# Performance work log

Hardware: AMD Instinct MI355X
Metric: run time of the kernel (lower is better)

The kernel has to match this reference:

```python
import jax, jax.numpy as jnp
import numpy as np
import math

V, BS, D, L, H = 50257, 1024, 768, 12, 4
DH = D // H  # 192
B, T = 4, 1024


def setup_inputs() -> dict:
    key = jax.random.key(0)
    ks = jax.random.split(key, 18)
    s = 0.02
    inp = {
        "x": jax.random.randint(ks[0], (B, T), 0, V),
        "tok_emb": jax.random.normal(ks[1], (V, D), jnp.float32) * s,
        "pos_emb": jax.random.normal(ks[2], (BS, D), jnp.float32) * s,
        "ln1_s": jnp.ones((L, D), jnp.float32),
        "ln1_b": jnp.zeros((L, D), jnp.float32),
        "qkv_w": jax.random.normal(ks[3], (L, D, 3 * D), jnp.float32) * s,
        "qkv_b": jnp.zeros((L, 3 * D), jnp.float32),
        "ln2_s": jnp.ones((L, D), jnp.float32),
        "ln2_b": jnp.zeros((L, D), jnp.float32),
        "fc_w": jax.random.normal(ks[4], (L, D, 4 * D), jnp.float32) * s,
        "fc_b": jnp.zeros((L, 4 * D), jnp.float32),
        "proj_w": jax.random.normal(ks[5], (L, 4 * D, D), jnp.float32) * s,
        "proj_b": jnp.zeros((L, D), jnp.float32),
        "lnf_s": jnp.ones((D,), jnp.float32),
        "lnf_b": jnp.zeros((D,), jnp.float32),
        "head_w": jax.random.normal(ks[6], (D, V), jnp.float32) * s,
        "head_b": jnp.zeros((V,), jnp.float32),
    }
    return inp


def _ln(x, scale, shift):
    m = x.mean(-1, keepdims=True)
    v = jnp.mean((x - m) ** 2, axis=-1, keepdims=True)
    return (x - m) * jax.lax.rsqrt(v + 1e-5) * scale + shift


def _forward(x, tok_emb, pos_emb, ln1_s, ln1_b, qkv_w, qkv_b, ln2_s, ln2_b,
             fc_w, fc_b, proj_w, proj_b, lnf_s, lnf_b, head_w, head_b):
    Bx, Tx = x.shape
    h = tok_emb[x] + pos_emb[:Tx]  # [B,T,D]
    causal = jnp.tril(jnp.ones((Tx, Tx), bool))
    scale = 1.0 / math.sqrt(DH)

    def block(h, p):
        s1, b1, wq, bq, s2, b2, wf, bf, wp, bp = p
        # attention (no output projection, faithful to source)
        ln1 = _ln(h, s1, b1)
        qkv = ln1 @ wq + bq  # [B,T,3D]
        q, k, v = jnp.split(qkv, 3, axis=-1)
        q = q.reshape(Bx, Tx, H, DH)
        k = k.reshape(Bx, Tx, H, DH)
        v = v.reshape(Bx, Tx, H, DH)
        att = jnp.einsum('bthd,bshd->bhts', q, k) * scale
        att = jnp.where(causal, att, -jnp.inf)
        att = jax.nn.softmax(att, axis=-1)
        y = jnp.einsum('bhts,bshd->bthd', att, v).reshape(Bx, Tx, D)
        h = h + y
        # MLP (ReLU, despite attr named gelu in source)
        ln2 = _ln(h, s2, b2)
        m = jax.nn.relu(ln2 @ wf + bf) @ wp + bp
        return h + m, None

    h, _ = jax.lax.scan(block, h,
                        (ln1_s, ln1_b, qkv_w, qkv_b, ln2_s, ln2_b,
                         fc_w, fc_b, proj_w, proj_b))
    h = _ln(h, lnf_s, lnf_b)
    return h @ head_w + head_b  # [B,T,V]


def reference(x, tok_emb, pos_emb, ln1_s, ln1_b, qkv_w, qkv_b, ln2_s, ln2_b,
              fc_w, fc_b, proj_w, proj_b, lnf_s, lnf_b, head_w, head_b):
    return _forward(x, tok_emb, pos_emb, ln1_s, ln1_b, qkv_w, qkv_b,
                    ln2_s, ln2_b, fc_w, fc_b, proj_w, proj_b,
                    lnf_s, lnf_b, head_w, head_b)
```

## Files before the change

### kernel.cpp

```cpp
#include <hip/hip_runtime.h>
#include <stdint.h>

#define D_MODEL 768
#define NHEAD 4
#define DHEAD 192
#define SEQ 1024
#define NLAYER 12
#define NTOK 4096
#define NVOCAB 50257

typedef __attribute__((ext_vector_type(4))) float f32x4;
typedef __attribute__((ext_vector_type(4))) int i32x4;
typedef __attribute__((ext_vector_type(4))) unsigned short u16x4;

__device__ __forceinline__ unsigned short f2bf(float f) {
  unsigned u = __builtin_bit_cast(unsigned, f);
  u += 0x7FFFu + ((u >> 16) & 1u);
  return (unsigned short)(u >> 16);
}

#define GLDS(src, dst)                                                   \
  __builtin_amdgcn_global_load_lds(                                      \
      (const __attribute__((address_space(1))) void*)(src),              \
      (__attribute__((address_space(3))) void*)(dst), 16, 0, 0)

__global__ __launch_bounds__(256) void embed_kernel(
    const int* __restrict__ x, const float* __restrict__ tok,
    const float* __restrict__ pos, float* __restrict__ h) {
  int row = blockIdx.x;
  int t = row & (SEQ - 1);
  int id = x[row];
  const float* tp = tok + (long)id * D_MODEL;
  const float* pp = pos + (long)t * D_MODEL;
  float* hp = h + (long)row * D_MODEL;
  for (int j = threadIdx.x; j < D_MODEL; j += 256)
    hp[j] = tp[j] + pp[j];
}

__global__ __launch_bounds__(256) void ln_kernel(
    const float* __restrict__ h, const float* __restrict__ sc,
    const float* __restrict__ sh, unsigned short* __restrict__ out) {
  __shared__ float red[4];
  int row = blockIdx.x;
  const float* x = h + (long)row * D_MODEL;
  int tid = threadIdx.x;
  float v0 = x[tid], v1 = x[tid + 256], v2 = x[tid + 512];
  float s = v0 + v1 + v2;
  for (int o = 32; o > 0; o >>= 1) s += __shfl_xor(s, o);
  if ((tid & 63) == 0) red[tid >> 6] = s;
  __syncthreads();
  float mean = (red[0] + red[1] + red[2] + red[3]) * (1.0f / D_MODEL);
  __syncthreads();
  float d0 = v0 - mean, d1 = v1 - mean, d2 = v2 - mean;
  float q = d0 * d0 + d1 * d1 + d2 * d2;
  for (int o = 32; o > 0; o >>= 1) q += __shfl_xor(q, o);
  if ((tid & 63) == 0) red[tid >> 6] = q;
  __syncthreads();
  float var = (red[0] + red[1] + red[2] + red[3]) * (1.0f / D_MODEL);
  float r = rsqrtf(var + 1e-5f);
  unsigned short* op = out + (long)row * D_MODEL;
  op[tid]       = f2bf(d0 * r * sc[tid]       + sh[tid]);
  op[tid + 256] = f2bf(d1 * r * sc[tid + 256] + sh[tid + 256]);
  op[tid + 512] = f2bf(d2 * r * sc[tid + 512] + sh[tid + 512]);
}

__global__ __launch_bounds__(256) void wtrans_kernel(
    const float* __restrict__ w, unsigned short* __restrict__ wt, int K, int N) {
  __shared__ unsigned short tile[32][33];
  int n0 = blockIdx.x * 32, k0 = blockIdx.y * 32;
  int tx = threadIdx.x, ty = threadIdx.y;
  int n = n0 + tx; if (n >= N) n = N - 1;
  #pragma unroll
  for (int i = 0; i < 4; ++i) {
    int k = k0 + ty + i * 8;
    tile[ty + i * 8][tx] = f2bf(w[(long)k * N + n]);
  }
  __syncthreads();
  #pragma unroll
  for (int i = 0; i < 4; ++i) {
    int nn = n0 + ty + i * 8;
    if (nn < N) wt[(long)nn * K + k0 + tx] = tile[tx][ty + i * 8];
  }
}

__global__ __launch_bounds__(256) void vt_kernel(
    const unsigned short* __restrict__ qkv, unsigned short* __restrict__ vt) {
  __shared__ unsigned short tile[32][33];
  int bh = blockIdx.z, b = bh >> 2, hh = bh & 3;
  int t0 = blockIdx.x * 32, f0 = blockIdx.y * 32;
  int tx = threadIdx.x, ty = threadIdx.y;
  const unsigned short* src = qkv + (long)b * SEQ * 2304 + 2 * D_MODEL + hh * DHEAD;
  #pragma unroll
  for (int i = 0; i < 4; ++i) {
    int t = t0 + ty + i * 8;
    tile[ty + i * 8][tx] = src[(long)t * 2304 + f0 + tx];
  }
  __syncthreads();
  unsigned short* dst = vt + (long)bh * DHEAD * SEQ;
  #pragma unroll
  for (int i = 0; i < 4; ++i) {
    int f = f0 + ty + i * 8;
    dst[(long)f * SEQ + t0 + tx] = tile[tx][ty + i * 8];
  }
}

__global__ __launch_bounds__(256) void softmax_kernel(
    const float* __restrict__ S, unsigned short* __restrict__ P) {
  __shared__ float red[4];
  long rid = blockIdx.x;
  int q = (int)(rid & (SEQ - 1));
  int tid = threadIdx.x;
  int i0 = tid * 4;
  f32x4 v = *(const f32x4*)(S + rid * SEQ + i0);
  float m = -3.0e38f;
  #pragma unroll
  for (int j = 0; j < 4; ++j) {
    if (i0 + j > q) v[j] = -3.0e38f;
    m = fmaxf(m, v[j]);
  }
  for (int o = 32; o > 0; o >>= 1) m = fmaxf(m, __shfl_xor(m, o));
  if ((tid & 63) == 0) red[tid >> 6] = m;
  __syncthreads();
  m = fmaxf(fmaxf(red[0], red[1]), fmaxf(red[2], red[3]));
  __syncthreads();
  float e[4];
  float sum = 0.f;
  #pragma unroll
  for (int j = 0; j < 4; ++j) {
    e[j] = (i0 + j > q) ? 0.f : __expf(v[j] - m);
    sum += e[j];
  }
  for (int o = 32; o > 0; o >>= 1) sum += __shfl_xor(sum, o);
  if ((tid & 63) == 0) red[tid >> 6] = sum;
  __syncthreads();
  float inv = 1.0f / (red[0] + red[1] + red[2] + red[3]);
  u16x4 out;
  #pragma unroll
  for (int j = 0; j < 4; ++j) out[j] = f2bf(e[j] * inv);
  *(u16x4*)(P + rid * SEQ + i0) = out;
}

#define BM 128
#define BN 128
#define BKK 32

template<int MODE>
__global__ __launch_bounds__(256) void gemm_kernel(
    const unsigned short* __restrict__ A, int lda,
    const unsigned short* __restrict__ B, int ldb,
    const float* __restrict__ bias,
    void* __restrict__ Cv, int ldc,
    int M, int N, int K,
    int NI, long sAo, long sAi, long sBo, long sBi,
    long sCo, long sCi, float alpha, int causal, int mblocks) {
  __shared__ __align__(16) unsigned short As[BM * BKK];
  __shared__ __align__(16) unsigned short Bs[BN * BKK];
  int z = blockIdx.z;
  int zo = z / NI, zi = z - zo * NI;
  A += zo * sAo + zi * sAi;
  B += zo * sBo + zi * sBi;
  long coff = zo * sCo + zi * sCi;

  int m0, n0;
  if (mblocks > 0) {
    int bid = blockIdx.x;
    int qq = (int)gridDim.x >> 3;
    bid = (bid & 7) * qq + (bid >> 3);
    m0 = (bid % mblocks) * BM;
    n0 = (bid / mblocks) * BN;
  } else {
    m0 = blockIdx.y * BM;
    n0 = blockIdx.x * BN;
  }
  if (causal == 1 && n0 > m0 + BM - 1) return;
  int kmax = (causal == 2) ? min(K, m0 + BM) : K;

  int tid = threadIdx.x;
  int lane = tid & 63;
  int wave = tid >> 6;
  int wm = (wave >> 1) * 64;
  int wn = (wave & 1) * 64;

  f32x4 acc[4][4] = {};

  for (int k0 = 0; k0 < kmax; k0 += BKK) {
    __syncthreads();
    #pragma unroll
    for (int i = 0; i < 2; ++i) {
      int c0 = i * 256 + wave * 64;
      int cc = c0 + lane;
      int row = cc >> 2;
      int ko = (cc & 3) << 3;
      GLDS(A + (long)(m0 + row) * lda + k0 + ko, As + c0 * 8);
      int rg = n0 + row; if (rg >= N) rg = N - 1;
      GLDS(B + (long)rg * ldb + k0 + ko, Bs + c0 * 8);
    }
    __syncthreads();
    int lr = lane & 15;
    int kg = (lane >> 4) << 3;
    i32x4 af[4], bf[4];
    #pragma unroll
    for (int mi = 0; mi < 4; ++mi)
      af[mi] = *(const i32x4*)(As + (wm + mi * 16 + lr) * BKK + kg);
    #pragma unroll
    for (int ni = 0; ni < 4; ++ni)
      bf[ni] = *(const i32x4*)(Bs + (wn + ni * 16 + lr) * BKK + kg);
    #pragma unroll
    for (int mi = 0; mi < 4; ++mi)
      #pragma unroll
      for (int ni = 0; ni < 4; ++ni)
        asm("v_mfma_f32_16x16x32_bf16 %0, %1, %2, %0"
            : "+v"(acc[mi][ni]) : "v"(af[mi]), "v"(bf[ni]));
  }

  int cr = (lane >> 4) << 2;
  int cn = lane & 15;
  #pragma unroll
  for (int mi = 0; mi < 4; ++mi) {
    #pragma unroll
    for (int ni = 0; ni < 4; ++ni) {
      int col = n0 + wn + ni * 16 + cn;
      if (col >= N) continue;
      float bv = (MODE == 2) ? 0.f : (bias ? bias[col] : 0.f);
      #pragma unroll
      for (int r = 0; r < 4; ++r) {
        long row = m0 + wm + mi * 16 + cr + r;
        float v = acc[mi][ni][r] * alpha + bv;
        long idx = coff + row * ldc + col;
        if (MODE == 0)      ((unsigned short*)Cv)[idx] = f2bf(v);
        else if (MODE == 1) ((unsigned short*)Cv)[idx] = f2bf(fmaxf(v, 0.f));
        else if (MODE == 2) ((float*)Cv)[idx] = v;
        else if (MODE == 3) ((float*)Cv)[idx] += v;
        else                ((float*)Cv)[idx] = v;
      }
    }
  }
}

extern "C" void kernel_launch(void* const* d_in, const int* in_sizes, int n_in,
                              void* d_out, int out_size, void* d_ws, size_t ws_size,
                              hipStream_t stream) {
  const int*   x       = (const int*)  d_in[0];
  const float* tok_emb = (const float*)d_in[1];
  const float* pos_emb = (const float*)d_in[2];
  const float* ln1_s   = (const float*)d_in[3];
  const float* ln1_b   = (const float*)d_in[4];
  const float* qkv_w   = (const float*)d_in[5];
  const float* qkv_b   = (const float*)d_in[6];
  const float* ln2_s   = (const float*)d_in[7];
  const float* ln2_b   = (const float*)d_in[8];
  const float* fc_w    = (const float*)d_in[9];
  const float* fc_b    = (const float*)d_in[10];
  const float* proj_w  = (const float*)d_in[11];
  const float* proj_b  = (const float*)d_in[12];
  const float* lnf_s   = (const float*)d_in[13];
  const float* lnf_b   = (const float*)d_in[14];
  const float* head_w  = (const float*)d_in[15];
  const float* head_b  = (const float*)d_in[16];

  char* ws = (char*)d_ws;
  size_t off = 0;
  auto alloc = [&](size_t bytes) {
    char* p = ws + off;
    off += (bytes + 255) & ~(size_t)255;
    return p;
  };
  float*          h   = (float*)         alloc((size_t)NTOK * D_MODEL * 4);
  unsigned short* lnb = (unsigned short*)alloc((size_t)NTOK * D_MODEL * 2);
  unsigned short* qkv = (unsigned short*)alloc((size_t)NTOK * 2304 * 2);
  unsigned short* vt  = (unsigned short*)alloc((size_t)16 * DHEAD * SEQ * 2);
  unsigned short* mid = (unsigned short*)alloc((size_t)NTOK * 3072 * 2);
  float*          S   = (float*)         alloc((size_t)16 * SEQ * SEQ * 4);
  unsigned short* P   = (unsigned short*)alloc((size_t)16 * SEQ * SEQ * 2);
  unsigned short* wtq = (unsigned short*)alloc((size_t)2304 * 768 * 2);
  unsigned short* wtf = (unsigned short*)alloc((size_t)3072 * 768 * 2);
  unsigned short* wtp = (unsigned short*)alloc((size_t)768 * 3072 * 2);
  unsigned short* wth = (unsigned short*)alloc((size_t)50304 * 768 * 2);

  embed_kernel<<<NTOK, 256, 0, stream>>>(x, tok_emb, pos_emb, h);

  const float rscale = 0.07216878364870323f;

  for (int l = 0; l < NLAYER; ++l) {
    wtrans_kernel<<<dim3(72, 24), dim3(32, 8), 0, stream>>>(
        qkv_w + (long)l * 768 * 2304, wtq, 768, 2304);
    ln_kernel<<<NTOK, 256, 0, stream>>>(h, ln1_s + l * 768, ln1_b + l * 768, lnb);
    gemm_kernel<0><<<dim3(18, 32, 1), 256, 0, stream>>>(
        lnb, 768, wtq, 768, qkv_b + l * 2304, qkv, 2304,
        4096, 2304, 768, 1, 0, 0, 0, 0, 0, 0, 1.0f, 0, 0);
    vt_kernel<<<dim3(32, 6, 16), dim3(32, 8), 0, stream>>>(qkv, vt);
    gemm_kernel<2><<<dim3(8, 8, 16), 256, 0, stream>>>(
        qkv, 2304, qkv + 768, 2304, nullptr, S, 1024,
        1024, 1024, 192, 4,
        (long)1024 * 2304, 192, (long)1024 * 2304, 192,
        (long)4 * 1024 * 1024, (long)1024 * 1024, rscale, 1, 0);
    softmax_kernel<<<16384, 256, 0, stream>>>(S, P);
    gemm_kernel<3><<<dim3(2, 8, 16), 256, 0, stream>>>(
        P, 1024, vt, 1024, nullptr, h, 768,
        1024, 192, 1024, 4,
        (long)4 * 1024 * 1024, (long)1024 * 1024,
        (long)4 * 192 * 1024, (long)192 * 1024,
        (long)1024 * 768, 192, 1.0f, 2, 0);
    wtrans_kernel<<<dim3(96, 24), dim3(32, 8), 0, stream>>>(
        fc_w + (long)l * 768 * 3072, wtf, 768, 3072);
    ln_kernel<<<NTOK, 256, 0, stream>>>(h, ln2_s + l * 768, ln2_b + l * 768, lnb);
    gemm_kernel<1><<<dim3(24, 32, 1), 256, 0, stream>>>(
        lnb, 768, wtf, 768, fc_b + l * 3072, mid, 3072,
        4096, 3072, 768, 1, 0, 0, 0, 0, 0, 0, 1.0f, 0, 0);
    wtrans_kernel<<<dim3(24, 96), dim3(32, 8), 0, stream>>>(
        proj_w + (long)l * 3072 * 768, wtp, 3072, 768);
    gemm_kernel<3><<<dim3(6, 32, 1), 256, 0, stream>>>(
        mid, 3072, wtp, 3072, proj_b + l * 768, h, 768,
        4096, 768, 3072, 1, 0, 0, 0, 0, 0, 0, 1.0f, 0, 0);
  }

  wtrans_kernel<<<dim3(1571, 24), dim3(32, 8), 0, stream>>>(head_w, wth, 768, 50257);
  ln_kernel<<<NTOK, 256, 0, stream>>>(h, lnf_s, lnf_b, lnb);
  gemm_kernel<4><<<dim3(393 * 32, 1, 1), 256, 0, stream>>>(
      lnb, 768, wth, 768, head_b, (float*)d_out, 50257,
      4096, 50257, 768, 1, 0, 0, 0, 0, 0, 0, 1.0f, 0, 32);
}
```

Before: 3.550 ms.

## Vectorize GEMM epilogue via swapped MFMA operands, skip masked softmax work, merge weight transposes

Swapping the MFMA A/B operands puts four consecutive output columns in each lane, so the epilogue can issue 16-byte float stores and 8-byte bf16 stores plus vector bias loads, where it used to write scalars with a row stride. The softmax kernel now skips loading fully masked score chunks and skips writing P tiles that lie entirely above the causal diagonal. The three per-layer weight transposes are merged into one launch to cut launch count. The wide epilogue loads and stores assume column offsets are aligned to four elements, which matters for the vocab-sized head output where N is odd.

```diff
diff --git a/kernel.cpp b/kernel.cpp
--- a/kernel.cpp
+++ b/kernel.cpp
@@ -64,6 +64,31 @@
   op[tid + 512] = f2bf(d2 * r * sc[tid + 512] + sh[tid + 512]);
 }
 
+__global__ __launch_bounds__(256) void wtrans3_kernel(
+    const float* __restrict__ qw, const float* __restrict__ fw,
+    const float* __restrict__ pw, unsigned short* __restrict__ tq,
+    unsigned short* __restrict__ tf, unsigned short* __restrict__ tp) {
+  __shared__ unsigned short tile[32][33];
+  int bid = blockIdx.x;
+  const float* src; unsigned short* dst; int K, N, nb;
+  if (bid < 1728)               { src = qw; dst = tq; K = 768;  N = 2304; nb = 72; }
+  else if ((bid -= 1728) < 2304){ src = fw; dst = tf; K = 768;  N = 3072; nb = 96; }
+  else { bid -= 2304;             src = pw; dst = tp; K = 3072; N = 768;  nb = 24; }
+  int n0 = (bid % nb) * 32, k0 = (bid / nb) * 32;
+  int tx = threadIdx.x & 31, ty = threadIdx.x >> 5;
+  #pragma unroll
+  for (int i = 0; i < 4; ++i) {
+    int k = k0 + ty + i * 8;
+    tile[ty + i * 8][tx] = f2bf(src[(long)k * N + n0 + tx]);
+  }
+  __syncthreads();
+  #pragma unroll
+  for (int i = 0; i < 4; ++i) {
+    int nn = n0 + ty + i * 8;
+    dst[(long)nn * K + k0 + tx] = tile[tx][ty + i * 8];
+  }
+}
+
 __global__ __launch_bounds__(256) void wtrans_kernel(
     const float* __restrict__ w, unsigned short* __restrict__ wt, int K, int N) {
   __shared__ unsigned short tile[32][33];
@@ -111,7 +136,12 @@
   int q = (int)(rid & (SEQ - 1));
   int tid = threadIdx.x;
   int i0 = tid * 4;
-  f32x4 v = *(const f32x4*)(S + rid * SEQ + i0);
+  f32x4 v;
+  if (i0 <= q) {
+    v = *(const f32x4*)(S + rid * SEQ + i0);
+  } else {
+    v = f32x4{-3.0e38f, -3.0e38f, -3.0e38f, -3.0e38f};
+  }
   float m = -3.0e38f;
   #pragma unroll
   for (int j = 0; j < 4; ++j) {
@@ -134,10 +164,12 @@
   if ((tid & 63) == 0) red[tid >> 6] = sum;
   __syncthreads();
   float inv = 1.0f / (red[0] + red[1] + red[2] + red[3]);
-  u16x4 out;
-  #pragma unroll
-  for (int j = 0; j < 4; ++j) out[j] = f2bf(e[j] * inv);
-  *(u16x4*)(P + rid * SEQ + i0) = out;
+  if ((i0 >> 7) <= (q >> 7)) {
+    u16x4 out;
+    #pragma unroll
+    for (int j = 0; j < 4; ++j) out[j] = f2bf(e[j] * inv);
+    *(u16x4*)(P + rid * SEQ + i0) = out;
+  }
 }
 
 #define BM 128
@@ -210,28 +242,58 @@
       #pragma unroll
       for (int ni = 0; ni < 4; ++ni)
         asm("v_mfma_f32_16x16x32_bf16 %0, %1, %2, %0"
-            : "+v"(acc[mi][ni]) : "v"(af[mi]), "v"(bf[ni]));
-  }
-
-  int cr = (lane >> 4) << 2;
-  int cn = lane & 15;
+            : "+v"(acc[mi][ni]) : "v"(bf[ni]), "v"(af[mi]));
+  }
+
+  int cm = lane & 15;
+  int cg = (lane >> 4) << 2;
   #pragma unroll
   for (int mi = 0; mi < 4; ++mi) {
+    long row = m0 + wm + mi * 16 + cm;
     #pragma unroll
     for (int ni = 0; ni < 4; ++ni) {
-      int col = n0 + wn + ni * 16 + cn;
-      if (col >= N) continue;
-      float bv = (MODE == 2) ? 0.f : (bias ? bias[col] : 0.f);
-      #pragma unroll
-      for (int r = 0; r < 4; ++r) {
-        long row = m0 + wm + mi * 16 + cr + r;
-        float v = acc[mi][ni][r] * alpha + bv;
-        long idx = coff + row * ldc + col;
-        if (MODE == 0)      ((unsigned short*)Cv)[idx] = f2bf(v);
-        else if (MODE == 1) ((unsigned short*)Cv)[idx] = f2bf(fmaxf(v, 0.f));
-        else if (MODE == 2) ((float*)Cv)[idx] = v;
-        else if (MODE == 3) ((float*)Cv)[idx] += v;
-        else                ((float*)Cv)[idx] = v;
+      int col = n0 + wn + ni * 16 + cg;
+      f32x4 v = acc[mi][ni];
+      if (MODE == 2) {
+        #pragma unroll
+        for (int r = 0; r < 4; ++r) v[r] *= alpha;
+        *(f32x4*)((float*)Cv + coff + row * (long)ldc + col) = v;
+      } else if (MODE == 0 || MODE == 1) {
+        f32x4 bv = *(const f32x4*)(bias + col);
+        u16x4 o;
+        #pragma unroll
+        for (int r = 0; r < 4; ++r) {
+          float t = v[r] + bv[r];
+          if (MODE == 1) t = fmaxf(t, 0.f);
+          o[r] = f2bf(t);
+        }
+        *(u16x4*)((unsigned short*)Cv + coff + row * (long)ldc + col) = o;
+      } else {
+        float* cp = (float*)Cv + coff + row * (long)ldc + col;
+        if (col + 4 <= N) {
+          f32x4 bv = bias ? *(const f32x4*)(bias + col)
+                          : f32x4{0.f, 0.f, 0.f, 0.f};
+          if (MODE == 3) {
+            f32x4 old = *(f32x4*)cp;
+            #pragma unroll
+            for (int r = 0; r < 4; ++r) old[r] += v[r] + bv[r];
+            *(f32x4*)cp = old;
+          } else {
+            f32x4 o;
+            #pragma unroll
+            for (int r = 0; r < 4; ++r) o[r] = v[r] + bv[r];
+            *(f32x4*)cp = o;
+          }
+        } else {
+          #pragma unroll
+          for (int r = 0; r < 4; ++r) {
+            if (col + r < N) {
+              float bvr = bias ? bias[col + r] : 0.f;
+              if (MODE == 3) cp[r] += v[r] + bvr;
+              else           cp[r] = v[r] + bvr;
+            }
+          }
+        }
       }
     }
   }
@@ -282,8 +344,9 @@
   const float rscale = 0.07216878364870323f;
 
   for (int l = 0; l < NLAYER; ++l) {
-    wtrans_kernel<<<dim3(72, 24), dim3(32, 8), 0, stream>>>(
-        qkv_w + (long)l * 768 * 2304, wtq, 768, 2304);
+    wtrans3_kernel<<<6336, 256, 0, stream>>>(
+        qkv_w + (long)l * 768 * 2304, fc_w + (long)l * 768 * 3072,
+        proj_w + (long)l * 3072 * 768, wtq, wtf, wtp);
     ln_kernel<<<NTOK, 256, 0, stream>>>(h, ln1_s + l * 768, ln1_b + l * 768, lnb);
     gemm_kernel<0><<<dim3(18, 32, 1), 256, 0, stream>>>(
         lnb, 768, wtq, 768, qkv_b + l * 2304, qkv, 2304,
@@ -301,14 +364,10 @@
         (long)4 * 1024 * 1024, (long)1024 * 1024,
         (long)4 * 192 * 1024, (long)192 * 1024,
         (long)1024 * 768, 192, 1.0f, 2, 0);
-    wtrans_kernel<<<dim3(96, 24), dim3(32, 8), 0, stream>>>(
-        fc_w + (long)l * 768 * 3072, wtf, 768, 3072);
     ln_kernel<<<NTOK, 256, 0, stream>>>(h, ln2_s + l * 768, ln2_b + l * 768, lnb);
     gemm_kernel<1><<<dim3(24, 32, 1), 256, 0, stream>>>(
         lnb, 768, wtf, 768, fc_b + l * 3072, mid, 3072,
         4096, 3072, 768, 1, 0, 0, 0, 0, 0, 0, 1.0f, 0, 0);
-    wtrans_kernel<<<dim3(24, 96), dim3(32, 8), 0, stream>>>(
-        proj_w + (long)l * 3072 * 768, wtp, 3072, 768);
     gemm_kernel<3><<<dim3(6, 32, 1), 256, 0, stream>>>(
         mid, 3072, wtp, 3072, proj_b + l * 768, h, 768,
         4096, 768, 3072, 1, 0, 0, 0, 0, 0, 0, 1.0f, 0, 0);
```

After: 3.355 ms. 1.06x faster.
